# Kernel tuning notes

Measured on AMD Instinct MI355X. Metric: run time of the kernel, lower is better.

## Reference

```python
import jax, jax.numpy as jnp
import numpy as np


def setup_inputs() -> dict:
    key = jax.random.key(0)
    ks = jax.random.split(key, 5)
    B, C, H, W = 8, 64, 64, 64
    Ci = 32  # inter_channels = in_channels // 2
    s = 1.0 / np.sqrt(C)
    return {
        "x": jax.random.normal(ks[0], (B, C, H, W), jnp.float32),
        "Wg": jax.random.normal(ks[1], (Ci, C), jnp.float32) * s,
        "bg": jnp.zeros((Ci,), jnp.float32),
        "Wt": jax.random.normal(ks[2], (Ci, C), jnp.float32) * s,
        "bt": jnp.zeros((Ci,), jnp.float32),
        "Wp": jax.random.normal(ks[3], (Ci, C), jnp.float32) * s,
        "bp": jnp.zeros((Ci,), jnp.float32),
        "Ww": jax.random.normal(ks[4], (C, Ci), jnp.float32) * (1.0 / np.sqrt(Ci)),
        "bw": jnp.zeros((C,), jnp.float32),
    }


def _proj(x, Wc, bc):
    # 1x1 conv: (B,C,H,W) -> (B,O,H,W), then flatten spatial -> (B,O,N)
    b, c, h, w = x.shape
    y = jnp.einsum("oc,bchw->bohw", Wc, x) + bc[None, :, None, None]
    return y.reshape(b, Wc.shape[0], h * w)


def reference(x, Wg, bg, Wt, bt, Wp, bp, Ww, bw):
    b, c, h, w = x.shape
    g_x = _proj(x, Wg, bg).transpose(0, 2, 1)      # (B, N, Ci)
    theta_x = _proj(x, Wt, bt).transpose(0, 2, 1)  # (B, N, Ci)
    phi_x = _proj(x, Wp, bp)                        # (B, Ci, N)
    f = jnp.einsum("bnd,bdm->bnm", theta_x, phi_x)  # (B, N, N)
    f_div_C = jax.nn.softmax(f, axis=-1)
    y = jnp.einsum("bnm,bmd->bnd", f_div_C, g_x)    # (B, N, Ci)
    y = y.transpose(0, 2, 1).reshape(b, Wg.shape[0], h, w)
    W_y = jnp.einsum("od,bdhw->bohw", Ww, y) + bw[None, :, None, None]
    return W_y + x
```

## Files before the change

kernel.cpp:

```cpp
#include <hip/hip_runtime.h>
#include <hip/hip_bf16.h>
#include <cstdint>
#include <cstddef>

#define B_ 8
#define C_ 64
#define CI 32
#define N_ 4096
#define LOG2E 1.44269504088896340736f

typedef __attribute__((ext_vector_type(8))) short bf16x8;
typedef __attribute__((ext_vector_type(4))) float f32x4;

static __device__ __forceinline__ ushort f2bf(float x) {
  union { float f; uint32_t u; } v; v.f = x;
  uint32_t r = v.u + 0x7FFFu + ((v.u >> 16) & 1u);
  return (ushort)(r >> 16);
}

static __device__ __forceinline__ uint32_t cvt_pk_bf16(float lo, float hi) {
  uint32_t r;
  asm("v_cvt_pk_bf16_f32 %0, %1, %2" : "=v"(r) : "v"(lo), "v"(hi));
  return r;
}

__global__ __launch_bounds__(256) void proj_kernel(
    const float* __restrict__ x,
    const float* __restrict__ Wg, const float* __restrict__ bg,
    const float* __restrict__ Wt, const float* __restrict__ bt,
    const float* __restrict__ Wp, const float* __restrict__ bp,
    ushort* __restrict__ theta_t, ushort* __restrict__ phi_t,
    ushort* __restrict__ gmat)
{
  const int z = blockIdx.z;
  const float* W; const float* bias;
  if (z == 0)      { W = Wt; bias = bt; }
  else if (z == 1) { W = Wp; bias = bp; }
  else             { W = Wg; bias = bg; }

  const int b = blockIdx.y;
  const int t = threadIdx.x;
  const int n = blockIdx.x * 64 + (t & 63);
  const int dq = t >> 6;
  const float* xb = x + ((size_t)b * C_) * N_ + n;
  const float* Wr = W + dq * 8 * C_;

  float acc[8];
  #pragma unroll
  for (int i = 0; i < 8; ++i) acc[i] = bias[dq * 8 + i];

  #pragma unroll 8
  for (int c = 0; c < C_; ++c) {
    const float xv = xb[(size_t)c * N_];
    #pragma unroll
    for (int i = 0; i < 8; ++i)
      acc[i] = fmaf(Wr[i * C_ + c], xv, acc[i]);
  }

  if (z == 2) {
    #pragma unroll
    for (int i = 0; i < 8; ++i)
      gmat[((size_t)(b * CI) + dq * 8 + i) * N_ + n] = f2bf(acc[i]);
  } else {
    const float scale = (z == 0) ? LOG2E : 1.0f;
    uint32_t w[4];
    #pragma unroll
    for (int k = 0; k < 4; ++k)
      w[k] = (uint32_t)f2bf(acc[2 * k] * scale) |
             ((uint32_t)f2bf(acc[2 * k + 1] * scale) << 16);
    ushort* base = (z == 0) ? theta_t : phi_t;
    *(uint4*)(base + ((size_t)(b * N_) + n) * CI + dq * 8) =
        make_uint4(w[0], w[1], w[2], w[3]);
  }
}

__global__ __launch_bounds__(256, 2) void attn_kernel(
    const ushort* __restrict__ theta_t,
    const ushort* __restrict__ phi_t,
    const ushort* __restrict__ gmat,
    const float* __restrict__ Ww, const float* __restrict__ bw,
    const float* __restrict__ x, float* __restrict__ out)
{
  __shared__ float scratch[2][64][40];
  __shared__ ushort Pt[4][2][16 * 64];
  __shared__ float WwL[C_ * CI];

  const int tid = threadIdx.x;
  const int lane = tid & 63;
  const int mh = tid >> 6;
  const int bid = blockIdx.x;
  const int b = bid & 7;
  const int n0 = (bid >> 3) * 64;
  const int g4 = lane >> 4;
  const int c16 = lane & 15;
  const int sw = (c16 & 7) << 4;

  #pragma unroll
  for (int i = 0; i < 8; ++i) WwL[tid + i * 256] = Ww[tid + i * 256];

  bf16x8 qfrag[4];
  #pragma unroll
  for (int s = 0; s < 4; ++s)
    qfrag[s] = *(const bf16x8*)(theta_t +
        ((size_t)(b * N_ + n0 + s * 16 + c16)) * CI + g4 * 8);

  f32x4 acc[4][2];
  #pragma unroll
  for (int s = 0; s < 4; ++s)
    #pragma unroll
    for (int dk = 0; dk < 2; ++dk) acc[s][dk] = (f32x4){0.f, 0.f, 0.f, 0.f};
  float m_run[4] = {0.f, 0.f, 0.f, 0.f};
  float l_lane[4] = {0.f, 0.f, 0.f, 0.f};

  const int mq0 = mh * 1024;
  const ushort* kbase = phi_t + ((size_t)(b * N_ + mq0 + c16)) * CI + g4 * 8;
  const ushort* vb0 = gmat + ((size_t)(b * CI + c16)) * N_ + mq0 + g4 * 8;
  const ushort* vb1 = vb0 + (size_t)16 * N_;

  char* pw[2][4]; const char* prd[2][2];
  #pragma unroll
  for (int pb = 0; pb < 2; ++pb) {
    #pragma unroll
    for (int mt = 0; mt < 4; ++mt)
      pw[pb][mt] = (char*)Pt[mh][pb] + ((c16 * 128 + mt * 32 + g4 * 8) ^ sw);
    #pragma unroll
    for (int ks = 0; ks < 2; ++ks)
      prd[pb][ks] = (const char*)Pt[mh][pb] + ((c16 * 128 + ks * 64 + g4 * 16) ^ sw);
  }

  bf16x8 kf[4];
  #pragma unroll
  for (int mt = 0; mt < 4; ++mt)
    kf[mt] = *(const bf16x8*)(kbase + (size_t)(mt * 16) * CI);

  const int NT = 16;
  for (int t = 0; t < NT; ++t) {
    bf16x8 vf0[2], vf1[2];
    #pragma unroll
    for (int ks = 0; ks < 2; ++ks) {
      vf0[ks] = *(const bf16x8*)(vb0 + t * 64 + ks * 32);
      vf1[ks] = *(const bf16x8*)(vb1 + t * 64 + ks * 32);
    }
    const int tn = (t + 1 < NT) ? t + 1 : t;
    bf16x8 kfn[4];
    #pragma unroll
    for (int mt = 0; mt < 4; ++mt)
      kfn[mt] = *(const bf16x8*)(kbase + (size_t)(tn * 64 + mt * 16) * CI);

    #pragma unroll
    for (int s = 0; s < 4; ++s) {
      const int pb = s & 1;
      f32x4 f[4];
      __builtin_amdgcn_s_setprio(1);
      #pragma unroll
      for (int mt = 0; mt < 4; ++mt)
        f[mt] = __builtin_amdgcn_mfma_f32_16x16x32_bf16(
            kf[mt], qfrag[s], (f32x4){0.f, 0.f, 0.f, 0.f}, 0, 0, 0);
      __builtin_amdgcn_s_setprio(0);

      float pm = -1e30f;
      float pv[4][4];
      #pragma unroll
      for (int mt = 0; mt < 4; ++mt) {
        #pragma unroll
        for (int r = 0; r < 4; ++r) {
          const float fv = f[mt][r];
          pm = fmaxf(pm, fv);
          pv[mt][r] = __builtin_amdgcn_exp2f(fv - m_run[s]);
        }
        l_lane[s] += (pv[mt][0] + pv[mt][1]) + (pv[mt][2] + pv[mt][3]);
      }
      #pragma unroll
      for (int mt = 0; mt < 4; ++mt) {
        uint2 wv;
        wv.x = cvt_pk_bf16(pv[mt][0], pv[mt][1]);
        wv.y = cvt_pk_bf16(pv[mt][2], pv[mt][3]);
        *(uint2*)pw[pb][mt] = wv;
      }
      asm volatile("s_waitcnt lgkmcnt(0)" ::: "memory");
      __builtin_amdgcn_sched_barrier(0);

      __builtin_amdgcn_s_setprio(1);
      #pragma unroll
      for (int ks = 0; ks < 2; ++ks) {
        const bf16x8 pfrag = *(const bf16x8*)prd[pb][ks];
        acc[s][0] = __builtin_amdgcn_mfma_f32_16x16x32_bf16(
            vf0[ks], pfrag, acc[s][0], 0, 0, 0);
        acc[s][1] = __builtin_amdgcn_mfma_f32_16x16x32_bf16(
            vf1[ks], pfrag, acc[s][1], 0, 0, 0);
      }
      __builtin_amdgcn_s_setprio(0);

      if (__any(pm > m_run[s] + 8.f)) {
        float pmr = fmaxf(pm, __shfl_xor(pm, 16));
        pmr = fmaxf(pmr, __shfl_xor(pmr, 32));
        const float mnew = fmaxf(m_run[s], pmr);
        const float sc = __builtin_amdgcn_exp2f(m_run[s] - mnew);
        m_run[s] = mnew;
        acc[s][0] *= sc; acc[s][1] *= sc; l_lane[s] *= sc;
      }
    }
    #pragma unroll
    for (int mt = 0; mt < 4; ++mt) kf[mt] = kfn[mt];
  }

  #pragma unroll
  for (int s = 0; s < 4; ++s) {
    l_lane[s] += __shfl_xor(l_lane[s], 16);
    l_lane[s] += __shfl_xor(l_lane[s], 32);
  }

  auto store_state = [&](float* sp) {
    #pragma unroll
    for (int s = 0; s < 4; ++s) {
      sp[s * 10 + 0] = m_run[s]; sp[s * 10 + 1] = l_lane[s];
      #pragma unroll
      for (int r = 0; r < 4; ++r) {
        sp[s * 10 + 2 + r] = acc[s][0][r];
        sp[s * 10 + 6 + r] = acc[s][1][r];
      }
    }
  };
  auto merge_state = [&](const float* sp) {
    #pragma unroll
    for (int s = 0; s < 4; ++s) {
      const float mb = sp[s * 10 + 0], lb = sp[s * 10 + 1];
      const float mM = fmaxf(m_run[s], mb);
      const float ea = __builtin_amdgcn_exp2f(m_run[s] - mM);
      const float eb = __builtin_amdgcn_exp2f(mb - mM);
      #pragma unroll
      for (int r = 0; r < 4; ++r) {
        acc[s][0][r] = acc[s][0][r] * ea + sp[s * 10 + 2 + r] * eb;
        acc[s][1][r] = acc[s][1][r] * ea + sp[s * 10 + 6 + r] * eb;
      }
      l_lane[s] = l_lane[s] * ea + lb * eb;
      m_run[s] = mM;
    }
  };

  if (mh == 1) store_state(scratch[0][lane]);
  if (mh == 3) store_state(scratch[1][lane]);
  __syncthreads();
  if (mh == 0) merge_state(scratch[0][lane]);
  if (mh == 2) merge_state(scratch[1][lane]);
  __syncthreads();
  if (mh == 2) store_state(scratch[0][lane]);
  __syncthreads();
  if (mh == 0) merge_state(scratch[0][lane]);
  __syncthreads();

  float* yl = &scratch[0][0][0];
  if (mh == 0) {
    #pragma unroll
    for (int s = 0; s < 4; ++s) {
      const float inv = 1.0f / l_lane[s];
      const int q = s * 16 + c16;
      #pragma unroll
      for (int r = 0; r < 4; ++r) {
        yl[(g4 * 4 + r) * 66 + q]      = acc[s][0][r] * inv;
        yl[(16 + g4 * 4 + r) * 66 + q] = acc[s][1][r] * inv;
      }
    }
  }
  __syncthreads();

  const int nl = tid & 63;
  const int cg = tid >> 6;
  float oacc[16];
  #pragma unroll
  for (int i = 0; i < 16; ++i) oacc[i] = bw[cg * 16 + i];
  #pragma unroll
  for (int d = 0; d < CI; ++d) {
    const float yv = yl[d * 66 + nl];
    #pragma unroll
    for (int i = 0; i < 16; ++i)
      oacc[i] = fmaf(WwL[(cg * 16 + i) * CI + d], yv, oacc[i]);
  }
  #pragma unroll
  for (int i = 0; i < 16; ++i) {
    const size_t idx = ((size_t)(b * C_ + cg * 16 + i)) * N_ + n0 + nl;
    out[idx] = oacc[i] + x[idx];
  }
}

extern "C" void kernel_launch(void* const* d_in, const int* in_sizes, int n_in,
                              void* d_out, int out_size, void* d_ws, size_t ws_size,
                              hipStream_t stream) {
  const float* x  = (const float*)d_in[0];
  const float* Wg = (const float*)d_in[1];
  const float* bg = (const float*)d_in[2];
  const float* Wt = (const float*)d_in[3];
  const float* bt = (const float*)d_in[4];
  const float* Wp = (const float*)d_in[5];
  const float* bp = (const float*)d_in[6];
  const float* Ww = (const float*)d_in[7];
  const float* bw = (const float*)d_in[8];
  float* out = (float*)d_out;

  char* ws = (char*)d_ws;
  ushort* theta_t = (ushort*)(ws);
  ushort* phi_t   = (ushort*)(ws + (size_t)2 * 1024 * 1024);
  ushort* gmat    = (ushort*)(ws + (size_t)4 * 1024 * 1024);

  proj_kernel<<<dim3(N_ / 64, B_, 3), 256, 0, stream>>>(
      x, Wg, bg, Wt, bt, Wp, bp, theta_t, phi_t, gmat);
  attn_kernel<<<dim3((N_ / 64) * B_), 256, 0, stream>>>(
      theta_t, phi_t, gmat, Ww, bw, x, out);
}
```

Baseline: 74.00 us.

## Split key range across eight waves per block with tree merge of softmax state

The attention block grows from 4 to 8 waves. Each wave now handles 512 keys instead of 1024, and the partial online-softmax states are combined in a log-depth shared-memory tree reduction. The next-tile key prefetch is removed, so key fragments are loaded at the top of each iteration. The aim is more waves in flight to hide latency across the 512 blocks, at the cost of more merge work, more barriers and higher LDS use.

```diff
diff --git a/kernel.cpp b/kernel.cpp
--- a/kernel.cpp
+++ b/kernel.cpp
@@ -74,16 +74,20 @@
   }
 }
 
-__global__ __launch_bounds__(256, 2) void attn_kernel(
+__global__ __launch_bounds__(512, 4) void attn_kernel(
     const ushort* __restrict__ theta_t,
     const ushort* __restrict__ phi_t,
     const ushort* __restrict__ gmat,
     const float* __restrict__ Ww, const float* __restrict__ bw,
     const float* __restrict__ x, float* __restrict__ out)
 {
-  __shared__ float scratch[2][64][40];
-  __shared__ ushort Pt[4][2][16 * 64];
+  __shared__ union {
+    ushort pt[8][2][16 * 64];
+    float  accS[4][32][64];
+  } Sh;
+  __shared__ float mlS[4][8][64];
   __shared__ float WwL[C_ * CI];
+  __shared__ float Yl[32 * 66];
 
   const int tid = threadIdx.x;
   const int lane = tid & 63;
@@ -96,7 +100,7 @@
   const int sw = (c16 & 7) << 4;
 
   #pragma unroll
-  for (int i = 0; i < 8; ++i) WwL[tid + i * 256] = Ww[tid + i * 256];
+  for (int i = 0; i < 4; ++i) WwL[tid + i * 512] = Ww[tid + i * 512];
 
   bf16x8 qfrag[4];
   #pragma unroll
@@ -106,13 +110,14 @@
 
   f32x4 acc[4][2];
   #pragma unroll
-  for (int s = 0; s < 4; ++s)
-    #pragma unroll
-    for (int dk = 0; dk < 2; ++dk) acc[s][dk] = (f32x4){0.f, 0.f, 0.f, 0.f};
+  for (int s = 0; s < 4; ++s) {
+    acc[s][0] = (f32x4){0.f, 0.f, 0.f, 0.f};
+    acc[s][1] = (f32x4){0.f, 0.f, 0.f, 0.f};
+  }
   float m_run[4] = {0.f, 0.f, 0.f, 0.f};
   float l_lane[4] = {0.f, 0.f, 0.f, 0.f};
 
-  const int mq0 = mh * 1024;
+  const int mq0 = mh * 512;
   const ushort* kbase = phi_t + ((size_t)(b * N_ + mq0 + c16)) * CI + g4 * 8;
   const ushort* vb0 = gmat + ((size_t)(b * CI + c16)) * N_ + mq0 + g4 * 8;
   const ushort* vb1 = vb0 + (size_t)16 * N_;
@@ -122,30 +127,25 @@
   for (int pb = 0; pb < 2; ++pb) {
     #pragma unroll
     for (int mt = 0; mt < 4; ++mt)
-      pw[pb][mt] = (char*)Pt[mh][pb] + ((c16 * 128 + mt * 32 + g4 * 8) ^ sw);
+      pw[pb][mt] = (char*)Sh.pt[mh][pb] + ((c16 * 128 + mt * 32 + g4 * 8) ^ sw);
     #pragma unroll
     for (int ks = 0; ks < 2; ++ks)
-      prd[pb][ks] = (const char*)Pt[mh][pb] + ((c16 * 128 + ks * 64 + g4 * 16) ^ sw);
-  }
-
-  bf16x8 kf[4];
-  #pragma unroll
-  for (int mt = 0; mt < 4; ++mt)
-    kf[mt] = *(const bf16x8*)(kbase + (size_t)(mt * 16) * CI);
-
-  const int NT = 16;
+      prd[pb][ks] = (const char*)Sh.pt[mh][pb] +
+                    ((c16 * 128 + ks * 64 + g4 * 16) ^ sw);
+  }
+
+  const int NT = 8;
   for (int t = 0; t < NT; ++t) {
+    bf16x8 kf[4];
+    #pragma unroll
+    for (int mt = 0; mt < 4; ++mt)
+      kf[mt] = *(const bf16x8*)(kbase + (size_t)(t * 64 + mt * 16) * CI);
     bf16x8 vf0[2], vf1[2];
     #pragma unroll
     for (int ks = 0; ks < 2; ++ks) {
       vf0[ks] = *(const bf16x8*)(vb0 + t * 64 + ks * 32);
       vf1[ks] = *(const bf16x8*)(vb1 + t * 64 + ks * 32);
     }
-    const int tn = (t + 1 < NT) ? t + 1 : t;
-    bf16x8 kfn[4];
-    #pragma unroll
-    for (int mt = 0; mt < 4; ++mt)
-      kfn[mt] = *(const bf16x8*)(kbase + (size_t)(tn * 64 + mt * 16) * CI);
 
     #pragma unroll
     for (int s = 0; s < 4; ++s) {
@@ -163,10 +163,10 @@
       #pragma unroll
       for (int mt = 0; mt < 4; ++mt) {
         #pragma unroll
-        for (int r = 0; r < 4; ++r) {
-          const float fv = f[mt][r];
+        for (int rr = 0; rr < 4; ++rr) {
+          const float fv = f[mt][rr];
           pm = fmaxf(pm, fv);
-          pv[mt][r] = __builtin_amdgcn_exp2f(fv - m_run[s]);
+          pv[mt][rr] = __builtin_amdgcn_exp2f(fv - m_run[s]);
         }
         l_lane[s] += (pv[mt][0] + pv[mt][1]) + (pv[mt][2] + pv[mt][3]);
       }
@@ -200,8 +200,6 @@
         acc[s][0] *= sc; acc[s][1] *= sc; l_lane[s] *= sc;
       }
     }
-    #pragma unroll
-    for (int mt = 0; mt < 4; ++mt) kf[mt] = kfn[mt];
   }
 
   #pragma unroll
@@ -210,55 +208,55 @@
     l_lane[s] += __shfl_xor(l_lane[s], 32);
   }
 
-  auto store_state = [&](float* sp) {
-    #pragma unroll
-    for (int s = 0; s < 4; ++s) {
-      sp[s * 10 + 0] = m_run[s]; sp[s * 10 + 1] = l_lane[s];
-      #pragma unroll
-      for (int r = 0; r < 4; ++r) {
-        sp[s * 10 + 2 + r] = acc[s][0][r];
-        sp[s * 10 + 6 + r] = acc[s][1][r];
-      }
-    }
-  };
-  auto merge_state = [&](const float* sp) {
-    #pragma unroll
-    for (int s = 0; s < 4; ++s) {
-      const float mb = sp[s * 10 + 0], lb = sp[s * 10 + 1];
-      const float mM = fmaxf(m_run[s], mb);
-      const float ea = __builtin_amdgcn_exp2f(m_run[s] - mM);
-      const float eb = __builtin_amdgcn_exp2f(mb - mM);
-      #pragma unroll
-      for (int r = 0; r < 4; ++r) {
-        acc[s][0][r] = acc[s][0][r] * ea + sp[s * 10 + 2 + r] * eb;
-        acc[s][1][r] = acc[s][1][r] * ea + sp[s * 10 + 6 + r] * eb;
-      }
-      l_lane[s] = l_lane[s] * ea + lb * eb;
-      m_run[s] = mM;
-    }
-  };
-
-  if (mh == 1) store_state(scratch[0][lane]);
-  if (mh == 3) store_state(scratch[1][lane]);
+  #pragma unroll
+  for (int r = 4; r >= 1; r >>= 1) {
+    __syncthreads();
+    if (mh >= r && mh < 2 * r) {
+      float* ad = &Sh.accS[mh - r][0][0] + lane;
+      float* md = &mlS[mh - r][0][0] + lane;
+      #pragma unroll
+      for (int s = 0; s < 4; ++s) {
+        #pragma unroll
+        for (int rr = 0; rr < 4; ++rr) {
+          ad[(s * 8 + rr) * 64]     = acc[s][0][rr];
+          ad[(s * 8 + 4 + rr) * 64] = acc[s][1][rr];
+        }
+        md[s * 64]       = m_run[s];
+        md[(4 + s) * 64] = l_lane[s];
+      }
+    }
+    __syncthreads();
+    if (mh < r) {
+      const float* as_ = &Sh.accS[mh][0][0] + lane;
+      const float* ms_ = &mlS[mh][0][0] + lane;
+      #pragma unroll
+      for (int s = 0; s < 4; ++s) {
+        const float mb = ms_[s * 64];
+        const float lb = ms_[(4 + s) * 64];
+        const float mM = fmaxf(m_run[s], mb);
+        const float ea = __builtin_amdgcn_exp2f(m_run[s] - mM);
+        const float eb = __builtin_amdgcn_exp2f(mb - mM);
+        #pragma unroll
+        for (int rr = 0; rr < 4; ++rr) {
+          acc[s][0][rr] = acc[s][0][rr] * ea + as_[(s * 8 + rr) * 64] * eb;
+          acc[s][1][rr] = acc[s][1][rr] * ea + as_[(s * 8 + 4 + rr) * 64] * eb;
+        }
+        l_lane[s] = l_lane[s] * ea + lb * eb;
+        m_run[s] = mM;
+      }
+    }
+  }
   __syncthreads();
-  if (mh == 0) merge_state(scratch[0][lane]);
-  if (mh == 2) merge_state(scratch[1][lane]);
-  __syncthreads();
-  if (mh == 2) store_state(scratch[0][lane]);
-  __syncthreads();
-  if (mh == 0) merge_state(scratch[0][lane]);
-  __syncthreads();
-
-  float* yl = &scratch[0][0][0];
+
   if (mh == 0) {
     #pragma unroll
     for (int s = 0; s < 4; ++s) {
       const float inv = 1.0f / l_lane[s];
       const int q = s * 16 + c16;
       #pragma unroll
-      for (int r = 0; r < 4; ++r) {
-        yl[(g4 * 4 + r) * 66 + q]      = acc[s][0][r] * inv;
-        yl[(16 + g4 * 4 + r) * 66 + q] = acc[s][1][r] * inv;
+      for (int rr = 0; rr < 4; ++rr) {
+        Yl[(g4 * 4 + rr) * 66 + q]      = acc[s][0][rr] * inv;
+        Yl[(16 + g4 * 4 + rr) * 66 + q] = acc[s][1][rr] * inv;
       }
     }
   }
@@ -266,19 +264,19 @@
 
   const int nl = tid & 63;
   const int cg = tid >> 6;
-  float oacc[16];
-  #pragma unroll
-  for (int i = 0; i < 16; ++i) oacc[i] = bw[cg * 16 + i];
+  float oacc[8];
+  #pragma unroll
+  for (int i = 0; i < 8; ++i) oacc[i] = bw[cg * 8 + i];
   #pragma unroll
   for (int d = 0; d < CI; ++d) {
-    const float yv = yl[d * 66 + nl];
-    #pragma unroll
-    for (int i = 0; i < 16; ++i)
-      oacc[i] = fmaf(WwL[(cg * 16 + i) * CI + d], yv, oacc[i]);
-  }
-  #pragma unroll
-  for (int i = 0; i < 16; ++i) {
-    const size_t idx = ((size_t)(b * C_ + cg * 16 + i)) * N_ + n0 + nl;
+    const float yv = Yl[d * 66 + nl];
+    #pragma unroll
+    for (int i = 0; i < 8; ++i)
+      oacc[i] = fmaf(WwL[(cg * 8 + i) * CI + d], yv, oacc[i]);
+  }
+  #pragma unroll
+  for (int i = 0; i < 8; ++i) {
+    const size_t idx = ((size_t)(b * C_ + cg * 8 + i)) * N_ + n0 + nl;
     out[idx] = oacc[i] + x[idx];
   }
 }
@@ -304,6 +302,6 @@
 
   proj_kernel<<<dim3(N_ / 64, B_, 3), 256, 0, stream>>>(
       x, Wg, bg, Wt, bt, Wp, bp, theta_t, phi_t, gmat);
-  attn_kernel<<<dim3((N_ / 64) * B_), 256, 0, stream>>>(
+  attn_kernel<<<dim3((N_ / 64) * B_), 512, 0, stream>>>(
       theta_t, phi_t, gmat, Ww, bw, x, out);
 }
```

Result: no change. 73.22 us (-1.1%).
